# Kernel optimization log

Measured on AMD Instinct MI355X. Metric: run time of the kernel, lower is better.

## Reference

```python
import jax, jax.numpy as jnp
import numpy as np

WS = 2   # window_size
NH = 8   # num_heads


def window_attn(x, Wqkv, bqkv, scale, ws=WS, nh=NH):
    # x: (B, H, W, C) -> tiny ws*ws-token windowed MHA, faithful to torch reshape order
    B, H, W, C = x.shape
    hg, wg = H // ws, W // ws
    hd = C // nh
    xw = x.reshape(B, hg, ws, wg, ws, C).transpose(0, 1, 3, 2, 4, 5)  # (B,hg,wg,ws,ws,C)
    qkv = (xw @ Wqkv + bqkv).reshape(B, hg * wg, ws * ws, 3, nh, hd)
    q, k, v = jnp.transpose(qkv, (3, 0, 1, 4, 2, 5))  # each (B,G,nh,n,hd), n=ws*ws
    attn = jax.nn.softmax(jnp.einsum('bgnqd,bgnkd->bgnqk', q, k) * scale, axis=-1)
    o = jnp.einsum('bgnqk,bgnkd->bgnqd', attn, v)
    o = o.transpose(0, 1, 3, 2, 4).reshape(B, hg, wg, ws, ws, C)
    return o.transpose(0, 1, 3, 2, 4, 5).reshape(B, H, W, C)


def reference(x, Wqkv, bqkv, Wproj, bproj):
    B, C, H, W = x.shape
    scale = (C // NH) ** (-0.5)
    xr = x.reshape(B, H, W, C)  # raw reshape (NOT a transpose) -- faithful to source

    # --- Global path ---
    g = window_attn(xr, Wqkv, bqkv, scale) @ Wproj + bproj

    # --- Local path ---
    l = xr.reshape(B, C, H, W)                         # raw reshape, as in source
    l = l.reshape(B, C, H // 2, 2, W // 2, 2).mean(axis=(3, 5))  # AvgPool2d(2)
    h, w = H // 2, W // 2
    l = l.reshape(B, h, w, C)                          # raw reshape, as in source
    l = window_attn(l, Wqkv, bqkv, scale)
    l = l.reshape(B, C, h, w)                          # raw reshape, as in source
    # attn_x: reflect-pad top by 1, AvgPool2d((2,1), stride=1)
    px = jnp.pad(l, ((0, 0), (0, 0), (1, 0), (0, 0)), mode='reflect')
    lx = 0.5 * (px[:, :, :-1, :] + px[:, :, 1:, :])
    # attn_y: reflect-pad right by 1, AvgPool2d((1,2), stride=1)
    py = jnp.pad(l, ((0, 0), (0, 0), (0, 0), (0, 1)), mode='reflect')
    ly = 0.5 * (py[..., :-1] + py[..., 1:])
    # bilinear upsample x2, align_corners=False (half-pixel, matches jax.image.resize)
    l = jax.image.resize(lx + ly, (B, C, H, W), method='bilinear')
    l = l.reshape(B, H, W, C)                          # raw reshape, as in source

    return (g + l).transpose(0, 3, 1, 2)  # (B, C, H, W)


def setup_inputs() -> dict:
    key = jax.random.key(0)
    k1, k2, k3, k4, k5 = jax.random.split(key, 5)
    B, C, H, W = 4, 512, 128, 128
    x = jax.random.normal(k1, (B, C, H, W), dtype=jnp.float32)
    Wqkv = jax.random.normal(k2, (C, 3 * C), dtype=jnp.float32) * 0.02
    bqkv = jax.random.normal(k3, (3 * C,), dtype=jnp.float32) * 0.02
    Wproj = jax.random.normal(k4, (C, C), dtype=jnp.float32) * 0.02
    bproj = jax.random.normal(k5, (C,), dtype=jnp.float32) * 0.02
    return {'x': x, 'Wqkv': Wqkv, 'bqkv': bqkv, 'Wproj': Wproj, 'bproj': bproj}
```

## Files before the change

### kernel.cpp

```cpp
#include <hip/hip_runtime.h>

typedef float f32x4 __attribute__((ext_vector_type(4)));
typedef float f32x2 __attribute__((ext_vector_type(2)));
typedef __bf16 bf16x8 __attribute__((ext_vector_type(8)));
typedef __bf16 bf16x4 __attribute__((ext_vector_type(4)));

__device__ __forceinline__ void gll16(const void* g, void* l) {
  __builtin_amdgcn_global_load_lds(
      (const __attribute__((address_space(1))) uint32_t*)g,
      (__attribute__((address_space(3))) uint32_t*)l, 16, 0, 0);
}

__global__ __launch_bounds__(256) void gemm_bf16_k512(
    const __bf16* __restrict__ A, const __bf16* __restrict__ BT,
    const float* __restrict__ bias, __bf16* __restrict__ C, int N)
{
  __shared__ __bf16 As[128 * 64];
  __shared__ __bf16 Bs[128 * 64];
  const int tid = threadIdx.x;
  const int wave = tid >> 6, lane = tid & 63;
  const int wr = (wave >> 1) * 64, wc = (wave & 1) * 64;
  const int l15 = lane & 15, l4 = lane >> 4;
  const long arow0 = (long)blockIdx.y * 128;
  const long brow0 = (long)blockIdx.x * 128;

  const int srow = wave * 8 + (lane >> 3);
  const int scp8 = (lane & 7) * 8;

  f32x4 acc[4][4] = {};

  for (int kt = 0; kt < 512; kt += 64) {
    #pragma unroll
    for (int i = 0; i < 4; i++) {
      int row = srow + i * 32;
      int gc = scp8 ^ ((row & 7) * 8);
      gll16(A  + (arow0 + row) * 512 + kt + gc, (char*)As + i * 4096 + wave * 1024);
      gll16(BT + (brow0 + row) * 512 + kt + gc, (char*)Bs + i * 4096 + wave * 1024);
    }
    __syncthreads();
    #pragma unroll
    for (int kk = 0; kk < 2; kk++) {
      bf16x8 af[4], bfr[4];
      #pragma unroll
      for (int m = 0; m < 4; m++) {
        int row = wr + m * 16 + l15;
        int cp8 = ((kk * 4 + l4) * 8) ^ ((row & 7) * 8);
        af[m] = *(const bf16x8*)&As[row * 64 + cp8];
      }
      #pragma unroll
      for (int n = 0; n < 4; n++) {
        int row = wc + n * 16 + l15;
        int cp8 = ((kk * 4 + l4) * 8) ^ ((row & 7) * 8);
        bfr[n] = *(const bf16x8*)&Bs[row * 64 + cp8];
      }
      #pragma unroll
      for (int m = 0; m < 4; m++)
        #pragma unroll
        for (int n = 0; n < 4; n++)
          acc[m][n] = __builtin_amdgcn_mfma_f32_16x16x32_bf16(af[m], bfr[n], acc[m][n], 0, 0, 0);
    }
    __syncthreads();
  }
  #pragma unroll
  for (int n = 0; n < 4; n++) {
    int col = (int)brow0 + wc + n * 16 + l15;
    float bv = bias[col];
    #pragma unroll
    for (int m = 0; m < 4; m++) {
      long row = arow0 + wr + m * 16 + l4 * 4;
      #pragma unroll
      for (int i = 0; i < 4; i++)
        C[(row + i) * (long)N + col] = (__bf16)(acc[m][n][i] + bv);
    }
  }
}

__global__ __launch_bounds__(256) void attn4(
    const __bf16* __restrict__ qkv, __bf16* __restrict__ o,
    int nwin, int wg, int Wimg, int wpb, int bst)
{
  int tid = blockIdx.x * 256 + threadIdx.x;
  int m = tid & 3;
  int head = (tid >> 2) & 7;
  int win = tid >> 5;
  if (win >= nwin) return;
  int b = win / wpb, wrm = win % wpb;
  int i = wrm / wg, j = wrm % wg;
  int t0 = b * bst + 2 * i * Wimg + 2 * j;
  int tn[4] = { t0, t0 + 1, t0 + Wimg, t0 + Wimg + 1 };
  int trow = tn[m];
  const int co = head * 64;

  float qf[64];
  #pragma unroll
  for (int c = 0; c < 8; c++) {
    bf16x8 v = *(const bf16x8*)(qkv + (long)trow * 1536 + co + c * 8);
    #pragma unroll
    for (int e = 0; e < 8; e++) qf[c * 8 + e] = (float)v[e];
  }

  float s[4];
  #pragma unroll
  for (int n = 0; n < 4; n++) {
    float acc = 0.f;
    #pragma unroll
    for (int c = 0; c < 8; c++) {
      bf16x8 kv = *(const bf16x8*)(qkv + (long)tn[n] * 1536 + 512 + co + c * 8);
      #pragma unroll
      for (int e = 0; e < 8; e++) acc += qf[c * 8 + e] * (float)kv[e];
    }
    s[n] = acc * 0.125f;
  }

  float mx = fmaxf(fmaxf(s[0], s[1]), fmaxf(s[2], s[3]));
  float e0 = __expf(s[0] - mx), e1 = __expf(s[1] - mx),
        e2 = __expf(s[2] - mx), e3 = __expf(s[3] - mx);
  float inv = 1.f / (e0 + e1 + e2 + e3);
  float w4[4] = { e0 * inv, e1 * inv, e2 * inv, e3 * inv };

  float of[64] = {};
  #pragma unroll
  for (int n = 0; n < 4; n++) {
    float wn = w4[n];
    #pragma unroll
    for (int c = 0; c < 8; c++) {
      bf16x8 vv = *(const bf16x8*)(qkv + (long)tn[n] * 1536 + 1024 + co + c * 8);
      #pragma unroll
      for (int e = 0; e < 8; e++) of[c * 8 + e] += wn * (float)vv[e];
    }
  }

  #pragma unroll
  for (int c = 0; c < 8; c++) {
    bf16x8 ov;
    #pragma unroll
    for (int e = 0; e < 8; e++) ov[e] = (__bf16)of[c * 8 + e];
    *(bf16x8*)(o + (long)trow * 512 + co + c * 8) = ov;
  }
}

__global__ __launch_bounds__(256) void transpose_f32_bf16(
    const float* __restrict__ in, __bf16* __restrict__ out, int K, int N)
{
  __shared__ float t[64][65];
  int n0 = blockIdx.x * 64, k0 = blockIdx.y * 64;
  int tid = threadIdx.x;
  int nl4 = (tid & 15) * 4, kl = tid >> 4;
  #pragma unroll
  for (int p = 0; p < 4; p++) {
    int kk = kl + p * 16;
    f32x4 v = *(const f32x4*)(in + (long)(k0 + kk) * N + n0 + nl4);
    t[kk][nl4 + 0] = v.x; t[kk][nl4 + 1] = v.y; t[kk][nl4 + 2] = v.z; t[kk][nl4 + 3] = v.w;
  }
  __syncthreads();
  int ks = tid & 63, wv = tid >> 6;
  #pragma unroll
  for (int p = 0; p < 16; p++) {
    int nn = wv * 16 + p;
    out[(long)(n0 + nn) * K + k0 + ks] = (__bf16)t[ks][nn];
  }
}

__global__ __launch_bounds__(256) void convpool(const float* __restrict__ x,
    __bf16* __restrict__ Xbf, __bf16* __restrict__ P)
{
  int t = blockIdx.x * 256 + threadIdx.x;
  int j8 = (t & 15) * 8;
  int i2 = (t >> 4) & 63;
  long bc = t >> 10;
  const float* r0 = x + bc * 16384 + (2 * i2) * 128 + j8;
  f32x4 a0 = *(const f32x4*)r0,         a1 = *(const f32x4*)(r0 + 4);
  f32x4 b0 = *(const f32x4*)(r0 + 128), b1 = *(const f32x4*)(r0 + 132);
  bf16x8 xa, xb;
  xa[0] = (__bf16)a0.x; xa[1] = (__bf16)a0.y; xa[2] = (__bf16)a0.z; xa[3] = (__bf16)a0.w;
  xa[4] = (__bf16)a1.x; xa[5] = (__bf16)a1.y; xa[6] = (__bf16)a1.z; xa[7] = (__bf16)a1.w;
  xb[0] = (__bf16)b0.x; xb[1] = (__bf16)b0.y; xb[2] = (__bf16)b0.z; xb[3] = (__bf16)b0.w;
  xb[4] = (__bf16)b1.x; xb[5] = (__bf16)b1.y; xb[6] = (__bf16)b1.z; xb[7] = (__bf16)b1.w;
  *(bf16x8*)(Xbf + bc * 16384 + (2 * i2) * 128 + j8) = xa;
  *(bf16x8*)(Xbf + bc * 16384 + (2 * i2) * 128 + 128 + j8) = xb;
  bf16x4 p;
  p[0] = (__bf16)((a0.x + a0.y + b0.x + b0.y) * 0.25f);
  p[1] = (__bf16)((a0.z + a0.w + b0.z + b0.w) * 0.25f);
  p[2] = (__bf16)((a1.x + a1.y + b1.x + b1.y) * 0.25f);
  p[3] = (__bf16)((a1.z + a1.w + b1.z + b1.w) * 0.25f);
  *(bf16x4*)(P + bc * 4096 + i2 * 64 + (t & 15) * 4) = p;
}

__global__ void skern(const __bf16* __restrict__ l, float* __restrict__ s)
{
  int tid = blockIdx.x * 256 + threadIdx.x;
  int j = tid & 63, i = (tid >> 6) & 63;
  long bc = tid >> 12;
  const __bf16* base = l + bc * 4096;
  int im1 = (i == 0) ? 1 : i - 1;
  int jp1 = (j == 63) ? 62 : j + 1;
  float v = 0.5f * (float)base[im1 * 64 + j] + (float)base[i * 64 + j]
          + 0.5f * (float)base[i * 64 + jp1];
  s[tid] = v;
}

__global__ __launch_bounds__(256) void final_v2(
    const __bf16* __restrict__ G, const float* __restrict__ S, float* __restrict__ out)
{
  __shared__ float Sl[8192];
  __shared__ float t[64][65];
  int b = blockIdx.z;
  int p0 = blockIdx.y * 64, c0 = blockIdx.x * 64;
  int tid = threadIdx.x;

  int k2 = blockIdx.y;
  const float* Sb = S + (long)b * 2097152 + (long)k2 * 8192;
  #pragma unroll
  for (int i = 0; i < 8; i++)
    *(f32x4*)&Sl[i * 1024 + tid * 4] = *(const f32x4*)(Sb + i * 1024 + tid * 4);
  __syncthreads();

  int cl4 = (tid & 15) * 4, pl = tid >> 4;
  const __bf16* Gb = G + ((long)b * 16384 + p0) * 512 + c0;
  #pragma unroll
  for (int q2 = 0; q2 < 4; q2++) {
    int pp = pl + q2 * 16;
    bf16x4 g = *(const bf16x4*)(Gb + (long)pp * 512 + cl4);
    int qbase = (p0 + pp) * 512 + c0 + cl4;
    #pragma unroll
    for (int e = 0; e < 4; e++) {
      int q = qbase + e;
      int lc = (q >> 14) & 1;
      int r = q & 16383, hh = r >> 7, ww = r & 127;
      const float* sb = Sl + lc * 4096;
      int i0, i1, j0, j1; float wi0, wi1, wj0, wj1;
      if (hh & 1) { i0 = hh >> 1; i1 = (i0 < 63) ? i0 + 1 : 63; wi0 = 0.75f; wi1 = 0.25f; }
      else        { i1 = hh >> 1; i0 = (i1 > 0) ? i1 - 1 : 0;   wi0 = 0.25f; wi1 = 0.75f; }
      if (ww & 1) { j0 = ww >> 1; j1 = (j0 < 63) ? j0 + 1 : 63; wj0 = 0.75f; wj1 = 0.25f; }
      else        { j1 = ww >> 1; j0 = (j1 > 0) ? j1 - 1 : 0;   wj0 = 0.25f; wj1 = 0.75f; }
      float up = wi0 * (wj0 * sb[i0 * 64 + j0] + wj1 * sb[i0 * 64 + j1])
               + wi1 * (wj0 * sb[i1 * 64 + j0] + wj1 * sb[i1 * 64 + j1]);
      t[pp][cl4 + e] = (float)g[e] + up;
    }
  }
  __syncthreads();
  int l15b = tid & 15, hi = (tid >> 4) & 3, wv = tid >> 6;
  float* ob = out + (long)b * 8388608 + (long)c0 * 16384 + p0;
  #pragma unroll
  for (int it = 0; it < 4; it++) {
    int cc = wv * 16 + it * 4 + hi;
    f32x4 v;
    v.x = t[l15b * 4 + 0][cc]; v.y = t[l15b * 4 + 1][cc];
    v.z = t[l15b * 4 + 2][cc]; v.w = t[l15b * 4 + 3][cc];
    *(f32x4*)(ob + (long)cc * 16384 + l15b * 4) = v;
  }
}

extern "C" void kernel_launch(void* const* d_in, const int* in_sizes, int n_in,
                              void* d_out, int out_size, void* d_ws, size_t ws_size,
                              hipStream_t stream)
{
  const float* x     = (const float*)d_in[0];
  const float* Wqkv  = (const float*)d_in[1];
  const float* bqkv  = (const float*)d_in[2];
  const float* Wproj = (const float*)d_in[3];
  const float* bproj = (const float*)d_in[4];
  float* out = (float*)d_out;

  char* w = (char*)d_ws;
  __bf16* WqkvT  = (__bf16*)w;  w += (size_t)1536 * 512 * 2;
  __bf16* WprojT = (__bf16*)w;  w += (size_t)512 * 512 * 2;
  __bf16* Xbf    = (__bf16*)w;  w += (size_t)65536 * 512 * 2;
  __bf16* G      = Xbf;
  __bf16* P      = (__bf16*)w;  w += (size_t)2048 * 4096 * 2;

  bool batched = ws_size >= ((size_t)356 << 20);
  size_t mchunk = batched ? 65536 : 16384;
  __bf16* QKVbuf = (__bf16*)w;  w += mchunk * 1536 * 2;
  __bf16* Obuf   = (__bf16*)w;
  float*  S      = (float*)QKVbuf;

  transpose_f32_bf16<<<dim3(24, 8), 256, 0, stream>>>(Wqkv, WqkvT, 512, 1536);
  transpose_f32_bf16<<<dim3(8, 8), 256, 0, stream>>>(Wproj, WprojT, 512, 512);
  convpool<<<8192, 256, 0, stream>>>(x, Xbf, P);

  int nch = batched ? 1 : 4;
  int mrows = (int)mchunk;
  for (int c = 0; c < nch; c++) {
    const __bf16* Ac = Xbf + (size_t)c * 16384 * 512;
    gemm_bf16_k512<<<dim3(12, mrows / 128), 256, 0, stream>>>(Ac, WqkvT, bqkv, QKVbuf, 1536);
    attn4<<<(mrows / 4) * 32 / 256, 256, 0, stream>>>(
        QKVbuf, Obuf, mrows / 4, 64, 128, 4096, 16384);
    gemm_bf16_k512<<<dim3(4, mrows / 128), 256, 0, stream>>>(Obuf, WprojT, bproj,
                                                             G + (size_t)c * 16384 * 512, 512);
  }

  gemm_bf16_k512<<<dim3(12, 128), 256, 0, stream>>>(P, WqkvT, bqkv, QKVbuf, 1536);
  attn4<<<512, 256, 0, stream>>>(QKVbuf, Obuf, 4096, 32, 64, 1024, 4096);
  skern<<<8388608 / 256, 256, 0, stream>>>(Obuf, S);

  final_v2<<<dim3(8, 256, 4), 256, 0, stream>>>(G, S, out);
}
```

Before: 481.1 us.

## Stage GEMM epilogue through swizzled LDS for coalesced stores and XCD-aware block remap

```diff
diff --git a/kernel.cpp b/kernel.cpp
--- a/kernel.cpp
+++ b/kernel.cpp
@@ -13,16 +13,21 @@
 
 __global__ __launch_bounds__(256) void gemm_bf16_k512(
     const __bf16* __restrict__ A, const __bf16* __restrict__ BT,
-    const float* __restrict__ bias, __bf16* __restrict__ C, int N)
-{
-  __shared__ __bf16 As[128 * 64];
-  __shared__ __bf16 Bs[128 * 64];
+    const float* __restrict__ bias, __bf16* __restrict__ C, int N, int gx)
+{
+  __shared__ __bf16 sh[16384];
+  __bf16* As = sh;
+  __bf16* Bs = sh + 8192;
   const int tid = threadIdx.x;
   const int wave = tid >> 6, lane = tid & 63;
   const int wr = (wave >> 1) * 64, wc = (wave & 1) * 64;
   const int l15 = lane & 15, l4 = lane >> 4;
-  const long arow0 = (long)blockIdx.y * 128;
-  const long brow0 = (long)blockIdx.x * 128;
+
+  int lin = blockIdx.x;
+  int olin = (lin & 7) * ((int)gridDim.x >> 3) + (lin >> 3);
+  int bn = olin % gx, bm = olin / gx;
+  const long arow0 = (long)bm * 128;
+  const long brow0 = (long)bn * 128;
 
   const int srow = wave * 8 + (lane >> 3);
   const int scp8 = (lane & 7) * 8;
@@ -57,20 +62,36 @@
       for (int m = 0; m < 4; m++)
         #pragma unroll
         for (int n = 0; n < 4; n++)
-          acc[m][n] = __builtin_amdgcn_mfma_f32_16x16x32_bf16(af[m], bfr[n], acc[m][n], 0, 0, 0);
+          acc[m][n] = __builtin_amdgcn_mfma_f32_16x16x32_bf16(bfr[n], af[m], acc[m][n], 0, 0, 0);
     }
     __syncthreads();
   }
+
   #pragma unroll
   for (int n = 0; n < 4; n++) {
-    int col = (int)brow0 + wc + n * 16 + l15;
-    float bv = bias[col];
+    f32x4 bv = *(const f32x4*)(bias + brow0 + wc + n * 16 + l4 * 4);
     #pragma unroll
     for (int m = 0; m < 4; m++) {
-      long row = arow0 + wr + m * 16 + l4 * 4;
-      #pragma unroll
-      for (int i = 0; i < 4; i++)
-        C[(row + i) * (long)N + col] = (__bf16)(acc[m][n][i] + bv);
+      int row = wr + m * 16 + l15;
+      int colb = (wc + n * 16 + l4 * 4) * 2;
+      int byte = row * 256 + (colb ^ ((row & 7) << 4));
+      bf16x4 o;
+      #pragma unroll
+      for (int k = 0; k < 4; k++) o[k] = (__bf16)(acc[m][n][k] + bv[k]);
+      *(bf16x4*)((char*)sh + byte) = o;
+    }
+  }
+  __syncthreads();
+  {
+    int row = tid >> 1;
+    int halfs = (tid & 1) * 8;
+    __bf16* gdst = C + (arow0 + row) * (long)N + brow0 + halfs * 8;
+    #pragma unroll
+    for (int k = 0; k < 8; k++) {
+      int s = halfs + k;
+      int slot = (s & 8) | ((s ^ row) & 7);
+      bf16x8 v = *(const bf16x8*)((const char*)sh + row * 256 + slot * 16);
+      *(bf16x8*)(gdst + k * 8) = v;
     }
   }
 }
@@ -283,14 +304,14 @@
   int mrows = (int)mchunk;
   for (int c = 0; c < nch; c++) {
     const __bf16* Ac = Xbf + (size_t)c * 16384 * 512;
-    gemm_bf16_k512<<<dim3(12, mrows / 128), 256, 0, stream>>>(Ac, WqkvT, bqkv, QKVbuf, 1536);
+    gemm_bf16_k512<<<12 * (mrows / 128), 256, 0, stream>>>(Ac, WqkvT, bqkv, QKVbuf, 1536, 12);
     attn4<<<(mrows / 4) * 32 / 256, 256, 0, stream>>>(
         QKVbuf, Obuf, mrows / 4, 64, 128, 4096, 16384);
-    gemm_bf16_k512<<<dim3(4, mrows / 128), 256, 0, stream>>>(Obuf, WprojT, bproj,
-                                                             G + (size_t)c * 16384 * 512, 512);
-  }
-
-  gemm_bf16_k512<<<dim3(12, 128), 256, 0, stream>>>(P, WqkvT, bqkv, QKVbuf, 1536);
+    gemm_bf16_k512<<<4 * (mrows / 128), 256, 0, stream>>>(
+        Obuf, WprojT, bproj, G + (size_t)c * 16384 * 512, 512, 4);
+  }
+
+  gemm_bf16_k512<<<12 * 128, 256, 0, stream>>>(P, WqkvT, bqkv, QKVbuf, 1536, 12);
   attn4<<<512, 256, 0, stream>>>(QKVbuf, Obuf, 4096, 32, 64, 1024, 4096);
   skern<<<8388608 / 256, 256, 0, stream>>>(Obuf, S);
 
```

After: 528.5 us. 1.1x slower.
